# Optimization experiments

Hardware: AMD Instinct MI355X
Metric: run time of the kernel (lower is better)

The kernel has to match this reference:

```python
import jax, jax.numpy as jnp
import numpy as np

B, T = 64, 524288          # batch, samples (~32.8 s @ 16 kHz)
D = 16                      # downsample_factor for the envelope follower
SR = 16000
EPS = 1e-7                  # avoids log10(0) in level detection


def _time_const(ms):
    # exp(-log10(9) / (sr * ms * 1e-3 * downsample_factor)), as in __init__
    return float(np.exp(-np.log10(9.0) / (SR * ms * 0.001 * D)))


def setup_inputs() -> dict:
    key = jax.random.key(0)
    audio = jax.random.normal(key, (B, T), dtype=jnp.float32) * 0.5
    return {
        "audio": audio,
        "threshold": jnp.float32(-30.0),               # dB
        "ratio": jnp.float32(4.0),
        "makeup": jnp.float32(6.0),                    # dB
        "attack_time": jnp.float32(_time_const(5.0)),
        "release_time": jnp.float32(_time_const(100.0)),
    }


def reference(audio, threshold, ratio, makeup, attack_time, release_time):
    # --- level detection in dB ---
    x_db = 20.0 * jnp.log10(jnp.abs(audio) + EPS)            # [B, T]
    # --- time-averaged downsampling by D (frame mean) ---
    x_db_ds = x_db.reshape(B, T // D, D).mean(axis=-1)       # [B, T//D]
    # --- static gain computer ---
    y_db = jnp.where(x_db_ds > threshold,
                     threshold + (x_db_ds - threshold) / ratio,
                     x_db_ds)
    g = y_db - x_db_ds                                       # desired gain in dB (<= 0)

    # --- attack/release envelope follower: sample-recurrent one-pole IIR ---
    def step(prev, g_t):
        alpha = jnp.where(g_t < prev, attack_time, release_time)
        new = alpha * prev + (1.0 - alpha) * g_t
        return new, new

    _, g_s = jax.lax.scan(step, jnp.zeros((B,), audio.dtype), g.T)  # [T//D, B]

    # --- upsample smoothed gain back to audio rate and apply with makeup ---
    gain = jnp.repeat(g_s.T, D, axis=1)                      # [B, T]
    return audio * jnp.power(jnp.float32(10.0), (gain + makeup) / 20.0)
```

## Files before the change

### kernel.cpp

```cpp
#include <hip/hip_runtime.h>

#define B_DIM 64
#define T_DIM 524288
#define D_FAC 16
#define LBLK 64
#define NB 512
#define NBLK_TOT 32768
#define CSTR 72
#define PF 8
#define EPSV 1e-7f
#define BIGC 1e30f

#define DB_PER_LOG2 6.0205999132796239f
#define L2TEN_OVER20 0.16609640474436813f

__device__ __forceinline__ float sum_log2_4(float4 x) {
  return __log2f(fabsf(x.x) + EPSV) + __log2f(fabsf(x.y) + EPSV) +
         __log2f(fabsf(x.z) + EPSV) + __log2f(fabsf(x.w) + EPSV);
}

template <int CTRL, int RM>
__device__ __forceinline__ float fmin_dpp_step(float v) {
  int vi = __float_as_int(v);
  int sh = __builtin_amdgcn_update_dpp(vi, vi, CTRL, RM, 0xf, false);
  return fminf(v, __int_as_float(sh));
}

__global__ __launch_bounds__(256) void k1_compose(
    const float* __restrict__ audio, const float* __restrict__ p_thr,
    const float* __restrict__ p_ratio, const float* __restrict__ p_att,
    const float* __restrict__ p_rel, float* __restrict__ consts) {
  const int tid = threadIdx.x;
  const int lane = tid & 63;
  const int w = tid >> 6;
  const int gblk = blockIdx.x * 4 + w;
  const int row = gblk >> 9;
  const int b = gblk & (NB - 1);
  const float thr = p_thr[0];
  const float A = p_att[0], R = p_rel[0];
  const float oneA = 1.f - A, oneR = 1.f - R;
  const float gslope = (1.f / p_ratio[0]) - 1.f;

  const size_t sbase = (size_t)row * T_DIM + (size_t)(b * LBLK + lane) * D_FAC;
  const float4* ap = (const float4*)(audio + sbase);
  float s = sum_log2_4(ap[0]) + sum_log2_4(ap[1]) + sum_log2_4(ap[2]) +
            sum_log2_4(ap[3]);
  float xdb = s * (DB_PER_LOG2 / 16.f);
  float g = fminf(0.f, (xdb - thr) * gslope);
  const int gi = __float_as_int(g);

  float c = (lane == 0) ? 0.f : BIGC;
  float c64 = BIGC;
#pragma unroll
  for (int t = 0; t < LBLK; ++t) {
    float gt = __int_as_float(__builtin_amdgcn_readlane(gi, t));
    float ca = oneA * gt, cr = oneR * gt;
    float prev = __int_as_float(__builtin_amdgcn_update_dpp(
        __float_as_int(BIGC), __float_as_int(c), 0x138 , 0xf,
        0xf, false));
    c64 = fminf(fmaf(A, c, ca), fmaf(R, c64, cr));
    c = fminf(fmaf(A, prev, ca), fmaf(R, c, cr));
  }
  float* outp = consts + (size_t)gblk * CSTR;
  outp[lane] = c;
  if (lane == 63) {
#pragma unroll
    for (int j = 0; j < 8; ++j) outp[64 + j] = c64;
  }
}

__global__ __launch_bounds__(64) void k2_scan(const float* __restrict__ consts,
                                              float* __restrict__ states,
                                              const float* __restrict__ p_att,
                                              const float* __restrict__ p_rel) {
  const int r = blockIdx.x;
  const int lane = threadIdx.x;
  const float A = p_att[0], R = p_rel[0];
  const int cls0 = (lane < 8) ? 8 * lane : 64;
  float s0 = 1.f;
  for (int i = 0; i < 64; ++i) s0 *= (i < cls0) ? A : R;
  const float rAR = A / R;
  const float sl0 = s0, sl1 = sl0 * rAR, sl2 = sl1 * rAR, sl3 = sl2 * rAR,
              sl4 = sl3 * rAR, sl5 = sl4 * rAR, sl6 = sl5 * rAR,
              sl7 = sl6 * rAR;

  const float* base = consts + (size_t)r * NB * CSTR;
  float* st = states + r * NB;
  const int loff = (lane < 8) ? 8 * lane : 64;

  float4 qa[PF], qb[PF];
#pragma unroll
  for (int u = 0; u < PF; ++u) {
    qa[u] = *(const float4*)(base + u * CSTR + loff);
    qb[u] = *(const float4*)(base + u * CSTR + loff + 4);
  }

  float p = 0.f;
  for (int j = 0; j < 8; ++j) {
    float sj = 0.f;
    for (int k = 0; k < 8; ++k) {
#pragma unroll
      for (int u = 0; u < PF; ++u) {
        const int b = j * 64 + k * PF + u;
        const int i = k * PF + u;
        float f0 = fmaf(sl0, p, qa[u].x);
        float f1 = fmaf(sl1, p, qa[u].y);
        float f2 = fmaf(sl2, p, qa[u].z);
        float f3 = fmaf(sl3, p, qa[u].w);
        float f4 = fmaf(sl4, p, qb[u].x);
        float f5 = fmaf(sl5, p, qb[u].y);
        float f6 = fmaf(sl6, p, qb[u].z);
        float f7 = fmaf(sl7, p, qb[u].w);
        float m = fminf(fminf(fminf(f0, f1), f2),
                        fminf(fminf(fminf(f3, f4), f5), fminf(f6, f7)));
        m = fmin_dpp_step<0x111, 0xf>(m);
        m = fmin_dpp_step<0x112, 0xf>(m);
        m = fmin_dpp_step<0x114, 0xf>(m);
        m = fmin_dpp_step<0x111, 0xf>(m);
        sj = (lane == i) ? p : sj;
        p = __int_as_float(__builtin_amdgcn_readlane(__float_as_int(m), 8));
        qa[u] = *(const float4*)(base + (b + PF) * CSTR + loff);
        qb[u] = *(const float4*)(base + (b + PF) * CSTR + loff + 4);
      }
    }
    st[j * 64 + lane] = sj;
  }
}

__global__ __launch_bounds__(256) void k3_apply(
    const float* __restrict__ audio, const float* __restrict__ states,
    const float* __restrict__ p_thr, const float* __restrict__ p_ratio,
    const float* __restrict__ p_makeup, const float* __restrict__ p_att,
    const float* __restrict__ p_rel, float* __restrict__ out) {
  const int tid = threadIdx.x;
  const int lane = tid & 63;
  const int w = tid >> 6;
  const int gblk = blockIdx.x * 4 + w;
  const int row = gblk >> 9;
  const int b = gblk & (NB - 1);
  const float thr = p_thr[0], ratio = p_ratio[0], mk = p_makeup[0];
  const float A = p_att[0], R = p_rel[0];
  const float oneA = 1.f - A, oneR = 1.f - R;
  const float gslope = (1.f / ratio) - 1.f;

  const size_t sbase = (size_t)row * T_DIM + (size_t)(b * LBLK + lane) * D_FAC;
  const float4* ap = (const float4*)(audio + sbase);
  float4 x0 = ap[0], x1 = ap[1], x2 = ap[2], x3 = ap[3];
  float s = sum_log2_4(x0) + sum_log2_4(x1) + sum_log2_4(x2) + sum_log2_4(x3);
  float xdb = s * (DB_PER_LOG2 / 16.f);
  float g = fminf(0.f, (xdb - thr) * gslope);

  float p = states[gblk];
  float m = 0.f;
  int gi = __float_as_int(g);
#pragma unroll
  for (int t = 0; t < LBLK; ++t) {
    float gt = __int_as_float(__builtin_amdgcn_readlane(gi, t));
    p = fminf(fmaf(A, p, oneA * gt), fmaf(R, p, oneR * gt));
    m = (lane == t) ? p : m;
  }
  float mult = exp2f((m + mk) * L2TEN_OVER20);
  float4* op = (float4*)(out + sbase);
  float4 y0, y1, y2, y3;
  y0.x = x0.x * mult; y0.y = x0.y * mult; y0.z = x0.z * mult; y0.w = x0.w * mult;
  y1.x = x1.x * mult; y1.y = x1.y * mult; y1.z = x1.z * mult; y1.w = x1.w * mult;
  y2.x = x2.x * mult; y2.y = x2.y * mult; y2.z = x2.z * mult; y2.w = x2.w * mult;
  y3.x = x3.x * mult; y3.y = x3.y * mult; y3.z = x3.z * mult; y3.w = x3.w * mult;
  op[0] = y0; op[1] = y1; op[2] = y2; op[3] = y3;
}

extern "C" void kernel_launch(void* const* d_in, const int* in_sizes, int n_in,
                              void* d_out, int out_size, void* d_ws,
                              size_t ws_size, hipStream_t stream) {
  const float* audio = (const float*)d_in[0];
  const float* thr = (const float*)d_in[1];
  const float* ratio = (const float*)d_in[2];
  const float* makeup = (const float*)d_in[3];
  const float* att = (const float*)d_in[4];
  const float* rel = (const float*)d_in[5];
  float* out = (float*)d_out;

  const size_t CONSTS_BYTES = (size_t)NBLK_TOT * CSTR * sizeof(float);
  const size_t PAD_BYTES = (size_t)PF * CSTR * sizeof(float);
  const size_t STATES_BYTES = (size_t)NBLK_TOT * sizeof(float);

  float* consts;
  float* states;
  if (ws_size >= CONSTS_BYTES + PAD_BYTES + STATES_BYTES) {
    consts = (float*)d_ws;
    states = (float*)((char*)d_ws + CONSTS_BYTES + PAD_BYTES);
  } else {
    consts = (float*)d_out;
    states = (float*)d_ws;
  }

  hipLaunchKernelGGL(k1_compose, dim3(8192), dim3(256), 0, stream, audio, thr,
                     ratio, att, rel, consts);
  hipLaunchKernelGGL(k2_scan, dim3(64), dim3(64), 0, stream, consts, states,
                     att, rel);
  hipLaunchKernelGGL(k3_apply, dim3(8192), dim3(256), 0, stream, audio, states,
                     thr, ratio, makeup, att, rel, out);
}
```

Measured before the change: 142.3 us.

## Stage scan coefficients through double-buffered LDS in sequential scan kernel

The serial scan kernel now loads each group of 64 blocks' composed coefficients with coalesced float4 loads into registers, then writes them to a double-buffered LDS array. The next group's global loads are issued while the current group is scanned. The per-step operand fetches inside the serial loop become LDS reads instead of strided global loads, which targets latency on the critical dependency chain. The host also always puts the coefficient buffer in the output array and drops the workspace-size branch, which removes the padding the old prefetch needed.

```diff
diff --git a/kernel.cpp b/kernel.cpp
--- a/kernel.cpp
+++ b/kernel.cpp
@@ -7,7 +7,7 @@
 #define NB 512
 #define NBLK_TOT 32768
 #define CSTR 72
-#define PF 8
+#define GRP 64
 #define EPSV 1e-7f
 #define BIGC 1e30f
 
@@ -73,6 +73,7 @@
                                               float* __restrict__ states,
                                               const float* __restrict__ p_att,
                                               const float* __restrict__ p_rel) {
+  __shared__ float sh[2][GRP * CSTR];
   const int r = blockIdx.x;
   const int lane = threadIdx.x;
   const float A = p_att[0], R = p_rel[0];
@@ -83,26 +84,41 @@
   const float sl0 = s0, sl1 = sl0 * rAR, sl2 = sl1 * rAR, sl3 = sl2 * rAR,
               sl4 = sl3 * rAR, sl5 = sl4 * rAR, sl6 = sl5 * rAR,
               sl7 = sl6 * rAR;
+  const int loff = (lane < 8) ? 8 * lane : 64;
 
   const float* base = consts + (size_t)r * NB * CSTR;
   float* st = states + r * NB;
-  const int loff = (lane < 8) ? 8 * lane : 64;
-
-  float4 qa[PF], qb[PF];
-#pragma unroll
-  for (int u = 0; u < PF; ++u) {
-    qa[u] = *(const float4*)(base + u * CSTR + loff);
-    qb[u] = *(const float4*)(base + u * CSTR + loff + 4);
+
+  float4 stg[18];
+  {
+    const float4* gsrc = (const float4*)base;
+#pragma unroll
+    for (int i = 0; i < 18; ++i) stg[i] = gsrc[i * 64 + lane];
+    float4* dst = (float4*)sh[0];
+#pragma unroll
+    for (int i = 0; i < 18; ++i) dst[i * 64 + lane] = stg[i];
   }
 
   float p = 0.f;
   for (int j = 0; j < 8; ++j) {
+    if (j < 7) {
+      const float4* gsrc = (const float4*)(base + (size_t)(j + 1) * GRP * CSTR);
+#pragma unroll
+      for (int i = 0; i < 18; ++i) stg[i] = gsrc[i * 64 + lane];
+    }
+
+    const float* buf = sh[j & 1];
     float sj = 0.f;
-    for (int k = 0; k < 8; ++k) {
-#pragma unroll
-      for (int u = 0; u < PF; ++u) {
-        const int b = j * 64 + k * PF + u;
-        const int i = k * PF + u;
+    float4 qa[4], qb[4];
+#pragma unroll
+    for (int u = 0; u < 4; ++u) {
+      qa[u] = *(const float4*)(buf + u * CSTR + loff);
+      qb[u] = *(const float4*)(buf + u * CSTR + loff + 4);
+    }
+    for (int k = 0; k < 16; ++k) {
+#pragma unroll
+      for (int u = 0; u < 4; ++u) {
+        const int i = k * 4 + u;
         float f0 = fmaf(sl0, p, qa[u].x);
         float f1 = fmaf(sl1, p, qa[u].y);
         float f2 = fmaf(sl2, p, qa[u].z);
@@ -119,11 +135,19 @@
         m = fmin_dpp_step<0x111, 0xf>(m);
         sj = (lane == i) ? p : sj;
         p = __int_as_float(__builtin_amdgcn_readlane(__float_as_int(m), 8));
-        qa[u] = *(const float4*)(base + (b + PF) * CSTR + loff);
-        qb[u] = *(const float4*)(base + (b + PF) * CSTR + loff + 4);
+        int nb = i + 4;
+        nb = (nb < GRP) ? nb : 0;
+        qa[u] = *(const float4*)(buf + nb * CSTR + loff);
+        qb[u] = *(const float4*)(buf + nb * CSTR + loff + 4);
       }
     }
     st[j * 64 + lane] = sj;
+
+    if (j < 7) {
+      float4* dst = (float4*)sh[(j + 1) & 1];
+#pragma unroll
+      for (int i = 0; i < 18; ++i) dst[i * 64 + lane] = stg[i];
+    }
   }
 }
 
@@ -180,19 +204,8 @@
   const float* rel = (const float*)d_in[5];
   float* out = (float*)d_out;
 
-  const size_t CONSTS_BYTES = (size_t)NBLK_TOT * CSTR * sizeof(float);
-  const size_t PAD_BYTES = (size_t)PF * CSTR * sizeof(float);
-  const size_t STATES_BYTES = (size_t)NBLK_TOT * sizeof(float);
-
-  float* consts;
-  float* states;
-  if (ws_size >= CONSTS_BYTES + PAD_BYTES + STATES_BYTES) {
-    consts = (float*)d_ws;
-    states = (float*)((char*)d_ws + CONSTS_BYTES + PAD_BYTES);
-  } else {
-    consts = (float*)d_out;
-    states = (float*)d_ws;
-  }
+  float* consts = (float*)d_out;
+  float* states = (float*)d_ws;
 
   hipLaunchKernelGGL(k1_compose, dim3(8192), dim3(256), 0, stream, audio, thr,
                      ratio, att, rel, consts);
```

Result: slower. 152.5 us (+7.1%).
